# Performance work log

Hardware: AMD Instinct MI355X
Metric: run time of the kernel (lower is better)

Reference implementation:

```python
import jax, jax.numpy as jnp
import numpy as np

N = 50000      # nodes
EPS = 1e-5     # BatchNorm eps


def setup_inputs() -> dict:
    key = jax.random.key(0)
    ks = jax.random.split(key, 8)
    F_IN, H, C, E = 128, 128, 40, 600000
    x = jax.random.normal(ks[0], (N, F_IN), jnp.float32)
    edge_index = jax.random.randint(ks[1], (2, E), 0, N, dtype=jnp.int64)
    def glorot(k, fi, fo):
        s = np.sqrt(6.0 / (fi + fo)).astype(np.float32)
        return jax.random.uniform(k, (fi, fo), jnp.float32, -s, s)
    return {
        "x": x, "edge_index": edge_index,
        "W1": glorot(ks[2], F_IN, H), "b1": jnp.zeros((H,), jnp.float32),
        "gamma1": jnp.ones((H,), jnp.float32), "beta1": jnp.zeros((H,), jnp.float32),
        "W2": glorot(ks[3], H, H), "b2": jnp.zeros((H,), jnp.float32),
        "gamma2": jnp.ones((H,), jnp.float32), "beta2": jnp.zeros((H,), jnp.float32),
        "W3": glorot(ks[4], H, C), "b3": jnp.zeros((C,), jnp.float32),
    }


def _gcn_conv(x, W, b, src, dst, norm):
    # X' = D^-1/2 (A+I) D^-1/2 (X W) + b   (PyG GCNConv with self-loops)
    h = x @ W                               # [N, Fo]
    msg = h[src] * norm[:, None]            # [E+N, Fo] gather + scale
    out = jax.ops.segment_sum(msg, dst, num_segments=N)  # scatter-add
    return out + b


def _batchnorm(x, gamma, beta):
    # training-mode BatchNorm1d: batch stats over node axis, biased variance
    mu = jnp.mean(x, axis=0)
    var = jnp.mean(jnp.square(x - mu), axis=0)
    return (x - mu) * jax.lax.rsqrt(var + EPS) * gamma + beta


def reference(x, edge_index, W1, b1, gamma1, beta1, W2, b2, gamma2, beta2, W3, b3):
    loops = jnp.arange(N, dtype=edge_index.dtype)
    src = jnp.concatenate([edge_index[0], loops])
    dst = jnp.concatenate([edge_index[1], loops])
    deg = jax.ops.segment_sum(jnp.ones_like(dst, dtype=x.dtype), dst, num_segments=N)
    dinv = jax.lax.rsqrt(jnp.maximum(deg, 1.0))  # deg >= 1 due to self-loops
    norm = dinv[src] * dinv[dst]                 # [E+N]

    h = _gcn_conv(x, W1, b1, src, dst, norm)
    h = jax.nn.relu(_batchnorm(h, gamma1, beta1))
    h = _gcn_conv(h, W2, b2, src, dst, norm)
    h = jax.nn.relu(_batchnorm(h, gamma2, beta2))
    h = _gcn_conv(h, W3, b3, src, dst, norm)
    return jax.nn.log_softmax(h, axis=-1)
```

## Files before the change

kernel.cpp:

```cpp
#include <hip/hip_runtime.h>
#include <hip/hip_bf16.h>

#define EPS 1e-5f
#define SCAN_BLOCKS 256

typedef __attribute__((ext_vector_type(8))) short bf16x8;
typedef __attribute__((ext_vector_type(4))) float f32x4;

__device__ inline float bf2f(unsigned short u) {
    union { unsigned int i; float f; } v;
    v.i = ((unsigned int)u) << 16;
    return v.f;
}

__device__ inline unsigned short f2bf(float f) {
    union { float f; unsigned int i; } v;
    v.f = f;
    unsigned int x = v.i;
    unsigned int rounded = x + 0x7FFF + ((x >> 16) & 1);
    return (unsigned short)(rounded >> 16);
}


__global__ void count_kernel(const int* __restrict__ dst, int* __restrict__ counts, int e) {
    int i = blockIdx.x * blockDim.x + threadIdx.x;
    if (i < e) atomicAdd(&counts[dst[i]], 1);
}

__global__ __launch_bounds__(256) void scan_partial_kernel(const int* __restrict__ counts,
                                                           int* __restrict__ partials, int n) {
    __shared__ int sh[256];
    int chunk = (n + gridDim.x - 1) / gridDim.x;
    int lo = blockIdx.x * chunk;
    int hi = lo + chunk; if (hi > n) hi = n;
    int s = 0;
    for (int i = lo + threadIdx.x; i < hi; i += 256) s += counts[i];
    sh[threadIdx.x] = s;
    __syncthreads();
    for (int d = 128; d; d >>= 1) {
        if (threadIdx.x < d) sh[threadIdx.x] += sh[threadIdx.x + d];
        __syncthreads();
    }
    if (threadIdx.x == 0) partials[blockIdx.x] = sh[0];
}

__global__ __launch_bounds__(256) void scan_level2_kernel(int* __restrict__ partials) {
    __shared__ int sh[256];
    int t = threadIdx.x;
    sh[t] = partials[t];
    __syncthreads();
    for (int d = 1; d < 256; d <<= 1) {
        int v = (t >= d) ? sh[t - d] : 0;
        __syncthreads();
        sh[t] += v;
        __syncthreads();
    }
    partials[t] = (t == 0) ? 0 : sh[t - 1];
}

__global__ __launch_bounds__(256) void scan_write_kernel(const int* __restrict__ counts,
                                                         const int* __restrict__ partials,
                                                         int* __restrict__ offs,
                                                         float* __restrict__ dinv, int n) {
    __shared__ int sh[256];
    int t = threadIdx.x;
    int chunk = (n + gridDim.x - 1) / gridDim.x;
    int lo = blockIdx.x * chunk;
    int hi = lo + chunk; if (hi > n) hi = n;
    int per = (chunk + 255) / 256;
    int tlo = lo + t * per;
    int thi = tlo + per; if (thi > hi) thi = hi;
    int s = 0;
    for (int i = tlo; i < thi; ++i) s += counts[i];
    sh[t] = s;
    __syncthreads();
    for (int d = 1; d < 256; d <<= 1) {
        int v = (t >= d) ? sh[t - d] : 0;
        __syncthreads();
        sh[t] += v;
        __syncthreads();
    }
    int run = partials[blockIdx.x] + ((t == 0) ? 0 : sh[t - 1]);
    for (int i = tlo; i < thi; ++i) {
        offs[i] = run;
        run += counts[i];
        dinv[i] = rsqrtf((float)(counts[i] + 1));
    }
    if (tlo < n && thi == n) offs[n] = run;
}

__global__ void scatter_kernel(const int* __restrict__ src, const int* __restrict__ dst,
                               const int* __restrict__ offs, int* __restrict__ fill,
                               const float* __restrict__ dinv,
                               int* __restrict__ csr_col, float* __restrict__ csr_val, int e) {
    int i = blockIdx.x * blockDim.x + threadIdx.x;
    if (i >= e) return;
    int s = src[i], d = dst[i];
    int pos = offs[d] + atomicAdd(&fill[d], 1);
    csr_col[pos] = s;
    csr_val[pos] = dinv[s] * dinv[d];
}

__global__ void prep_weights_kernel(const float* __restrict__ W1, const float* __restrict__ W2,
                                    const float* __restrict__ W3,
                                    unsigned short* __restrict__ WT1,
                                    unsigned short* __restrict__ WT2,
                                    unsigned short* __restrict__ WT3) {
    int i = blockIdx.x * blockDim.x + threadIdx.x;
    if (i < 16384) {
        int col = i >> 7, k = i & 127;
        WT1[i] = f2bf(W1[k * 128 + col]);
    } else if (i < 32768) {
        int j = i - 16384;
        int col = j >> 7, k = j & 127;
        WT2[j] = f2bf(W2[k * 128 + col]);
    } else if (i < 32768 + 6144) {
        int j = i - 32768;
        int col = j >> 7, k = j & 127;
        WT3[j] = (col < 40) ? f2bf(W3[k * 40 + col]) : 0;
    }
}

template<bool BN>
__global__ __launch_bounds__(256) void gemm128_mfma_kernel(
    const float* __restrict__ A, const unsigned short* __restrict__ WT,
    const float* __restrict__ stats, const float* __restrict__ gamma,
    const float* __restrict__ beta, float invn,
    unsigned short* __restrict__ C, int n) {
    __shared__ unsigned short lW[128 * 128];
    __shared__ unsigned short lA[64 * 128];
    int tid = threadIdx.x;
    const uint4* wsrc = (const uint4*)WT;
#pragma unroll
    for (int it = 0; it < 8; ++it) {
        int idx = tid + it * 256;
        int byte = idx << 4;
        int dst = byte ^ (((byte >> 8) & 7) << 4);
        *(uint4*)((char*)lW + dst) = wsrc[idx];
    }
    int row0 = blockIdx.x * 64;
#pragma unroll
    for (int it = 0; it < 4; ++it) {
        int idx = tid + it * 256;
        int r = idx >> 4;
        int cc = (idx & 15) << 3;
        int gr = row0 + r; if (gr > n - 1) gr = n - 1;
        const float* ap = A + (size_t)gr * 128 + cc;
        float4 f0 = *(const float4*)ap;
        float4 f1 = *(const float4*)(ap + 4);
        float v[8] = {f0.x, f0.y, f0.z, f0.w, f1.x, f1.y, f1.z, f1.w};
        union { unsigned short u[8]; uint4 q; } t;
#pragma unroll
        for (int j = 0; j < 8; ++j) {
            float x = v[j];
            if (BN) {
                int c = cc + j;
                float mu = stats[c] * invn;
                float var = stats[128 + c] * invn - mu * mu;
                float sc = gamma[c] * rsqrtf(var + EPS);
                float sh = beta[c] - mu * sc;
                x = fmaf(x, sc, sh);
                x = x > 0.0f ? x : 0.0f;
            }
            t.u[j] = f2bf(x);
        }
        int byte = idx << 4;
        int dst = byte ^ (((byte >> 8) & 7) << 4);
        *(uint4*)((char*)lA + dst) = t.q;
    }
    __syncthreads();

    int lane = tid & 63;
    int mrow0 = (tid >> 6) << 4;
    int arow = mrow0 + (lane & 15);
    int swz = (lane & 7) << 4;
    int koff = (lane >> 4) << 4;
    const char* pA = (const char*)lA + (arow << 8);
    const char* pB = (const char*)lW + ((lane & 15) << 8);
    f32x4 acc[8];
#pragma unroll
    for (int t8 = 0; t8 < 8; ++t8) acc[t8] = (f32x4){0.f, 0.f, 0.f, 0.f};
#pragma unroll
    for (int kk = 0; kk < 4; ++kk) {
        int kb = (kk << 6) + koff;
        bf16x8 af = *(const bf16x8*)(pA + (kb ^ swz));
#pragma unroll
        for (int t8 = 0; t8 < 8; ++t8) {
            bf16x8 bf = *(const bf16x8*)(pB + (t8 << 12) + (kb ^ swz));
            acc[t8] = __builtin_amdgcn_mfma_f32_16x16x32_bf16(af, bf, acc[t8], 0, 0, 0);
        }
    }
    int crow = row0 + mrow0 + ((lane >> 4) << 2);
    int ccol = lane & 15;
    unsigned short* cp = C + (size_t)crow * 128 + ccol;
#pragma unroll
    for (int j = 0; j < 4; ++j) {
        if (crow + j < n) {
#pragma unroll
            for (int t8 = 0; t8 < 8; ++t8)
                cp[(size_t)j * 128 + t8 * 16] = f2bf(acc[t8][j]);
        }
    }
}

__global__ __launch_bounds__(256) void gemm40_lsm_mfma_kernel(
    const unsigned short* __restrict__ A, const unsigned short* __restrict__ WT,
    const float* __restrict__ b3, float* __restrict__ out, int n) {
    __shared__ unsigned short lW[48 * 128];
    __shared__ unsigned short lA[64 * 128];
    __shared__ float sRow[64 * 49];
    __shared__ float sD[64];
    __shared__ float sB[48];
    int tid = threadIdx.x;
    if (tid < 48) sB[tid] = (tid < 40) ? b3[tid] : 0.0f;
    const uint4* wsrc = (const uint4*)WT;
#pragma unroll
    for (int it = 0; it < 3; ++it) {
        int idx = tid + it * 256;
        int byte = idx << 4;
        int dst = byte ^ (((byte >> 8) & 7) << 4);
        *(uint4*)((char*)lW + dst) = wsrc[idx];
    }
    int row0 = blockIdx.x * 64;
#pragma unroll
    for (int it = 0; it < 4; ++it) {
        int idx = tid + it * 256;
        int r = idx >> 4;
        int cc = (idx & 15) << 3;
        int gr = row0 + r; if (gr > n - 1) gr = n - 1;
        uint4 q = *(const uint4*)(A + (size_t)gr * 128 + cc);
        int byte = idx << 4;
        int dst = byte ^ (((byte >> 8) & 7) << 4);
        *(uint4*)((char*)lA + dst) = q;
    }
    __syncthreads();

    int lane = tid & 63;
    int mrow0 = (tid >> 6) << 4;
    int arow = mrow0 + (lane & 15);
    int swz = (lane & 7) << 4;
    int koff = (lane >> 4) << 4;
    const char* pA = (const char*)lA + (arow << 8);
    const char* pB = (const char*)lW + ((lane & 15) << 8);
    f32x4 acc[3];
#pragma unroll
    for (int t8 = 0; t8 < 3; ++t8) acc[t8] = (f32x4){0.f, 0.f, 0.f, 0.f};
#pragma unroll
    for (int kk = 0; kk < 4; ++kk) {
        int kb = (kk << 6) + koff;
        bf16x8 af = *(const bf16x8*)(pA + (kb ^ swz));
#pragma unroll
        for (int t8 = 0; t8 < 3; ++t8) {
            bf16x8 bf = *(const bf16x8*)(pB + (t8 << 12) + (kb ^ swz));
            acc[t8] = __builtin_amdgcn_mfma_f32_16x16x32_bf16(af, bf, acc[t8], 0, 0, 0);
        }
    }
    int lrow = mrow0 + ((lane >> 4) << 2);
    int ccol = lane & 15;
#pragma unroll
    for (int t8 = 0; t8 < 3; ++t8)
#pragma unroll
        for (int j = 0; j < 4; ++j)
            sRow[(lrow + j) * 49 + t8 * 16 + ccol] = acc[t8][j] + sB[t8 * 16 + ccol];
    __syncthreads();
    if (tid < 64) {
        float m = -1e30f;
        for (int c = 0; c < 40; ++c) m = fmaxf(m, sRow[tid * 49 + c]);
        float l = 0.0f;
        for (int c = 0; c < 40; ++c) l += expf(sRow[tid * 49 + c] - m);
        sD[tid] = m + logf(l);
    }
    __syncthreads();
    for (int i = tid; i < 64 * 40; i += 256) {
        int r = i / 40;
        int c = i - r * 40;
        int gr = row0 + r;
        if (gr < n) out[(size_t)gr * 40 + c] = sRow[r * 49 + c] - sD[r];
    }
}


template<bool OUT16>
__global__ __launch_bounds__(256) void aggregate128_kernel(
    const unsigned short* __restrict__ H, const int* __restrict__ offs,
    const int* __restrict__ cols, const float* __restrict__ vals,
    const float* __restrict__ dinv, void* __restrict__ outp, int n) {
    int node = (blockIdx.x * blockDim.x + threadIdx.x) >> 6;
    if (node >= n) return;
    int lane = threadIdx.x & 63;
    float di = dinv[node];
    unsigned int h0 = *(const unsigned int*)(H + (size_t)node * 128 + lane * 2);
    float2 acc0, acc1;
    acc0.x = bf2f((unsigned short)h0) * di * di;
    acc0.y = bf2f((unsigned short)(h0 >> 16)) * di * di;
    acc1.x = 0.0f; acc1.y = 0.0f;
    int e0 = offs[node], e1 = offs[node + 1];
    int e = e0;
    for (; e + 2 <= e1; e += 2) {
        int sA = cols[e], sB = cols[e + 1];
        float wA = vals[e], wB = vals[e + 1];
        unsigned int hA = *(const unsigned int*)(H + (size_t)sA * 128 + lane * 2);
        unsigned int hB = *(const unsigned int*)(H + (size_t)sB * 128 + lane * 2);
        acc0.x += bf2f((unsigned short)hA) * wA;
        acc0.y += bf2f((unsigned short)(hA >> 16)) * wA;
        acc1.x += bf2f((unsigned short)hB) * wB;
        acc1.y += bf2f((unsigned short)(hB >> 16)) * wB;
    }
    if (e < e1) {
        int sA = cols[e];
        float wA = vals[e];
        unsigned int hA = *(const unsigned int*)(H + (size_t)sA * 128 + lane * 2);
        acc0.x += bf2f((unsigned short)hA) * wA;
        acc0.y += bf2f((unsigned short)(hA >> 16)) * wA;
    }
    acc0.x += acc1.x;
    acc0.y += acc1.y;
    if (OUT16) {
        unsigned int pack = (unsigned int)f2bf(acc0.x) | ((unsigned int)f2bf(acc0.y) << 16);
        *(unsigned int*)((unsigned short*)outp + (size_t)node * 128 + lane * 2) = pack;
    } else {
        *(float2*)((float*)outp + (size_t)node * 128 + lane * 2) = acc0;
    }
}


__global__ __launch_bounds__(256) void bn_stats_kernel(const float* __restrict__ X,
                                                       float* __restrict__ stats, int n) {
    int tid = threadIdx.x;
    int c = tid & 127;
    int r0 = blockIdx.x * 2 + (tid >> 7);
    float s = 0.0f, q = 0.0f;
    for (int r = r0; r < n; r += gridDim.x * 2) {
        float v = X[(size_t)r * 128 + c];
        s += v;
        q += v * v;
    }
    __shared__ float sh[256], shq[256];
    sh[tid] = s; shq[tid] = q;
    __syncthreads();
    if (tid < 128) {
        atomicAdd(&stats[c], sh[tid] + sh[tid + 128]);
        atomicAdd(&stats[128 + c], shq[tid] + shq[tid + 128]);
    }
}

__global__ void bn_apply_relu_bf16_kernel(const float* __restrict__ X,
                                          const float* __restrict__ stats,
                                          const float* __restrict__ gamma,
                                          const float* __restrict__ beta,
                                          unsigned short* __restrict__ Y, int n, float invn) {
    int i = blockIdx.x * blockDim.x + threadIdx.x;
    int total = n * 32;
    if (i >= total) return;
    int c0 = (i & 31) * 4;
    float4 x = ((const float4*)X)[i];
    float xv[4] = {x.x, x.y, x.z, x.w};
    ushort4 o;
    unsigned short ov[4];
#pragma unroll
    for (int j = 0; j < 4; ++j) {
        int c = c0 + j;
        float mu = stats[c] * invn;
        float var = stats[128 + c] * invn - mu * mu;
        float sc = gamma[c] * rsqrtf(var + EPS);
        float sh = beta[c] - mu * sc;
        float v = fmaf(xv[j], sc, sh);
        ov[j] = f2bf(v > 0.0f ? v : 0.0f);
    }
    o.x = ov[0]; o.y = ov[1]; o.z = ov[2]; o.w = ov[3];
    ((ushort4*)Y)[i] = o;
}


extern "C" void kernel_launch(void* const* d_in, const int* in_sizes, int n_in,
                              void* d_out, int out_size, void* d_ws, size_t ws_size,
                              hipStream_t stream) {
    const float* x   = (const float*)d_in[0];
    const int*   ei  = (const int*)d_in[1];
    const float* W1  = (const float*)d_in[2];
    const float* g1  = (const float*)d_in[4];
    const float* bt1 = (const float*)d_in[5];
    const float* W2  = (const float*)d_in[6];
    const float* g2  = (const float*)d_in[8];
    const float* bt2 = (const float*)d_in[9];
    const float* W3  = (const float*)d_in[10];
    const float* b3  = (const float*)d_in[11];

    int n = in_sizes[0] / 128;
    int e = in_sizes[1] / 2;
    const int* src = ei;
    const int* dst = ei + e;

    char* p = (char*)d_ws;
    auto alloc = [&](size_t bytes) -> char* {
        char* q = p;
        p += (bytes + 255) & ~(size_t)255;
        return q;
    };
    int*            counts   = (int*)alloc((size_t)n * 4);
    int*            offs     = (int*)alloc((size_t)(n + 1) * 4);
    int*            fill     = (int*)alloc((size_t)n * 4);
    float*          dinv     = (float*)alloc((size_t)n * 4);
    int*            partials = (int*)alloc(SCAN_BLOCKS * 4);
    int*            csr_col  = (int*)alloc((size_t)e * 4);
    float*          csr_val  = (float*)alloc((size_t)e * 4);
    float*          stats    = (float*)alloc(512 * 4);
    unsigned short* WT1      = (unsigned short*)alloc(16384 * 2);
    unsigned short* WT2      = (unsigned short*)alloc(16384 * 2);
    unsigned short* WT3      = (unsigned short*)alloc(6144 * 2);
    unsigned short* Hb       = (unsigned short*)alloc((size_t)n * 128 * 2);
    unsigned short* Hb2      = (unsigned short*)alloc((size_t)n * 128 * 2);
    float*          bufA     = (float*)alloc((size_t)n * 128 * 4);

    hipMemsetAsync(counts, 0, (size_t)n * 4, stream);
    hipMemsetAsync(fill, 0, (size_t)n * 4, stream);
    hipMemsetAsync(stats, 0, 512 * 4, stream);

    const int tb = 256;
    float invn = 1.0f / n;
    prep_weights_kernel<<<(38912 + tb - 1) / tb, tb, 0, stream>>>(W1, W2, W3, WT1, WT2, WT3);
    count_kernel<<<(e + tb - 1) / tb, tb, 0, stream>>>(dst, counts, e);
    scan_partial_kernel<<<SCAN_BLOCKS, tb, 0, stream>>>(counts, partials, n);
    scan_level2_kernel<<<1, tb, 0, stream>>>(partials);
    scan_write_kernel<<<SCAN_BLOCKS, tb, 0, stream>>>(counts, partials, offs, dinv, n);
    scatter_kernel<<<(e + tb - 1) / tb, tb, 0, stream>>>(src, dst, offs, fill, dinv,
                                                         csr_col, csr_val, e);

    int gblocks = (n + 63) / 64;
    int ablocks = (n + 3) / 4;

    gemm128_mfma_kernel<false><<<gblocks, tb, 0, stream>>>(x, WT1, nullptr, nullptr, nullptr,
                                                           0.0f, Hb, n);
    aggregate128_kernel<false><<<ablocks, tb, 0, stream>>>(Hb, offs, csr_col, csr_val, dinv,
                                                           bufA, n);
    bn_stats_kernel<<<256, tb, 0, stream>>>(bufA, stats, n);
    gemm128_mfma_kernel<true><<<gblocks, tb, 0, stream>>>(bufA, WT2, stats, g1, bt1, invn,
                                                          Hb, n);
    aggregate128_kernel<false><<<ablocks, tb, 0, stream>>>(Hb, offs, csr_col, csr_val, dinv,
                                                           bufA, n);
    bn_stats_kernel<<<256, tb, 0, stream>>>(bufA, stats + 256, n);
    bn_apply_relu_bf16_kernel<<<(n * 32 + tb - 1) / tb, tb, 0, stream>>>(bufA, stats + 256, g2,
                                                                         bt2, Hb, n, invn);
    aggregate128_kernel<true><<<ablocks, tb, 0, stream>>>(Hb, offs, csr_col, csr_val, dinv,
                                                          Hb2, n);
    gemm40_lsm_mfma_kernel<<<gblocks, tb, 0, stream>>>(Hb2, WT3, b3, (float*)d_out, n);
}
```

Before: 305.9 us.

## Store aggregates as bf16, fuse BN-apply into aggregation, pack CSR col/val

Aggregation outputs are now written as bf16 instead of fp32, which halves the intermediate traffic read by bn_stats and the GEMM. The second BN+ReLU is fused into the third aggregation's gather, so the separate bn_apply kernel is removed. CSR column and weight are packed into int2 so one load fetches both, and the gather loop is unrolled by four with more accumulators. The BN scale and shift are precomputed once per block in shared memory; the cost is BN statistics computed on bf16-rounded values and BN math repeated on every neighbour gather.

```diff
diff --git a/kernel.cpp b/kernel.cpp
--- a/kernel.cpp
+++ b/kernel.cpp
@@ -92,13 +92,13 @@
 __global__ void scatter_kernel(const int* __restrict__ src, const int* __restrict__ dst,
                                const int* __restrict__ offs, int* __restrict__ fill,
                                const float* __restrict__ dinv,
-                               int* __restrict__ csr_col, float* __restrict__ csr_val, int e) {
+                               int2* __restrict__ csr, int e) {
     int i = blockIdx.x * blockDim.x + threadIdx.x;
     if (i >= e) return;
     int s = src[i], d = dst[i];
     int pos = offs[d] + atomicAdd(&fill[d], 1);
-    csr_col[pos] = s;
-    csr_val[pos] = dinv[s] * dinv[d];
+    float w = dinv[s] * dinv[d];
+    csr[pos] = make_int2(s, __float_as_int(w));
 }
 
 __global__ void prep_weights_kernel(const float* __restrict__ W1, const float* __restrict__ W2,
@@ -121,15 +121,26 @@
     }
 }
 
-template<bool BN>
+template<int MODE>
 __global__ __launch_bounds__(256) void gemm128_mfma_kernel(
-    const float* __restrict__ A, const unsigned short* __restrict__ WT,
+    const void* __restrict__ Aptr, const unsigned short* __restrict__ WT,
     const float* __restrict__ stats, const float* __restrict__ gamma,
     const float* __restrict__ beta, float invn,
     unsigned short* __restrict__ C, int n) {
     __shared__ unsigned short lW[128 * 128];
     __shared__ unsigned short lA[64 * 128];
+    __shared__ float scs[128], shs[128];
     int tid = threadIdx.x;
+    if (MODE == 1) {
+        if (tid < 128) {
+            float mu = stats[tid] * invn;
+            float var = stats[128 + tid] * invn - mu * mu;
+            float sc = gamma[tid] * rsqrtf(var + EPS);
+            scs[tid] = sc;
+            shs[tid] = beta[tid] - mu * sc;
+        }
+        __syncthreads();
+    }
     const uint4* wsrc = (const uint4*)WT;
 #pragma unroll
     for (int it = 0; it < 8; ++it) {
@@ -145,24 +156,25 @@
         int r = idx >> 4;
         int cc = (idx & 15) << 3;
         int gr = row0 + r; if (gr > n - 1) gr = n - 1;
-        const float* ap = A + (size_t)gr * 128 + cc;
-        float4 f0 = *(const float4*)ap;
-        float4 f1 = *(const float4*)(ap + 4);
-        float v[8] = {f0.x, f0.y, f0.z, f0.w, f1.x, f1.y, f1.z, f1.w};
         union { unsigned short u[8]; uint4 q; } t;
-#pragma unroll
-        for (int j = 0; j < 8; ++j) {
-            float x = v[j];
-            if (BN) {
+        if (MODE == 0) {
+            const float* ap = (const float*)Aptr + (size_t)gr * 128 + cc;
+            float4 f0 = *(const float4*)ap;
+            float4 f1 = *(const float4*)(ap + 4);
+            float v[8] = {f0.x, f0.y, f0.z, f0.w, f1.x, f1.y, f1.z, f1.w};
+#pragma unroll
+            for (int j = 0; j < 8; ++j) t.u[j] = f2bf(v[j]);
+        } else {
+            uint4 q = *(const uint4*)((const unsigned short*)Aptr + (size_t)gr * 128 + cc);
+            unsigned int w[4] = {q.x, q.y, q.z, q.w};
+#pragma unroll
+            for (int j = 0; j < 8; ++j) {
+                float x = bf2f((unsigned short)(w[j >> 1] >> ((j & 1) * 16)));
                 int c = cc + j;
-                float mu = stats[c] * invn;
-                float var = stats[128 + c] * invn - mu * mu;
-                float sc = gamma[c] * rsqrtf(var + EPS);
-                float sh = beta[c] - mu * sc;
-                x = fmaf(x, sc, sh);
+                x = fmaf(x, scs[c], shs[c]);
                 x = x > 0.0f ? x : 0.0f;
+                t.u[j] = f2bf(x);
             }
-            t.u[j] = f2bf(x);
         }
         int byte = idx << 4;
         int dst = byte ^ (((byte >> 8) & 7) << 4);
@@ -280,58 +292,77 @@
 }
 
 
-template<bool OUT16>
+template<bool BN>
 __global__ __launch_bounds__(256) void aggregate128_kernel(
     const unsigned short* __restrict__ H, const int* __restrict__ offs,
-    const int* __restrict__ cols, const float* __restrict__ vals,
-    const float* __restrict__ dinv, void* __restrict__ outp, int n) {
+    const int2* __restrict__ csr, const float* __restrict__ dinv,
+    const float* __restrict__ stats, const float* __restrict__ gamma,
+    const float* __restrict__ beta, float invn,
+    unsigned short* __restrict__ out, int n) {
     int node = (blockIdx.x * blockDim.x + threadIdx.x) >> 6;
     if (node >= n) return;
     int lane = threadIdx.x & 63;
+    int c0 = lane * 2;
+    float sc0 = 1.0f, sh0 = 0.0f, sc1 = 1.0f, sh1 = 0.0f;
+    if (BN) {
+        float mu0 = stats[c0] * invn;
+        float var0 = stats[128 + c0] * invn - mu0 * mu0;
+        sc0 = gamma[c0] * rsqrtf(var0 + EPS);
+        sh0 = beta[c0] - mu0 * sc0;
+        float mu1 = stats[c0 + 1] * invn;
+        float var1 = stats[128 + c0 + 1] * invn - mu1 * mu1;
+        sc1 = gamma[c0 + 1] * rsqrtf(var1 + EPS);
+        sh1 = beta[c0 + 1] - mu1 * sc1;
+    }
+    auto loadf = [&](int row) -> float2 {
+        unsigned int hv = *(const unsigned int*)(H + (size_t)row * 128 + c0);
+        float x0 = bf2f((unsigned short)hv);
+        float x1 = bf2f((unsigned short)(hv >> 16));
+        if (BN) {
+            x0 = fmaf(x0, sc0, sh0); x0 = x0 > 0.0f ? x0 : 0.0f;
+            x1 = fmaf(x1, sc1, sh1); x1 = x1 > 0.0f ? x1 : 0.0f;
+        }
+        return make_float2(x0, x1);
+    };
     float di = dinv[node];
-    unsigned int h0 = *(const unsigned int*)(H + (size_t)node * 128 + lane * 2);
-    float2 acc0, acc1;
-    acc0.x = bf2f((unsigned short)h0) * di * di;
-    acc0.y = bf2f((unsigned short)(h0 >> 16)) * di * di;
-    acc1.x = 0.0f; acc1.y = 0.0f;
-    int e0 = offs[node], e1 = offs[node + 1];
-    int e = e0;
-    for (; e + 2 <= e1; e += 2) {
-        int sA = cols[e], sB = cols[e + 1];
-        float wA = vals[e], wB = vals[e + 1];
-        unsigned int hA = *(const unsigned int*)(H + (size_t)sA * 128 + lane * 2);
-        unsigned int hB = *(const unsigned int*)(H + (size_t)sB * 128 + lane * 2);
-        acc0.x += bf2f((unsigned short)hA) * wA;
-        acc0.y += bf2f((unsigned short)(hA >> 16)) * wA;
-        acc1.x += bf2f((unsigned short)hB) * wB;
-        acc1.y += bf2f((unsigned short)(hB >> 16)) * wB;
-    }
-    if (e < e1) {
-        int sA = cols[e];
-        float wA = vals[e];
-        unsigned int hA = *(const unsigned int*)(H + (size_t)sA * 128 + lane * 2);
-        acc0.x += bf2f((unsigned short)hA) * wA;
-        acc0.y += bf2f((unsigned short)(hA >> 16)) * wA;
-    }
-    acc0.x += acc1.x;
-    acc0.y += acc1.y;
-    if (OUT16) {
-        unsigned int pack = (unsigned int)f2bf(acc0.x) | ((unsigned int)f2bf(acc0.y) << 16);
-        *(unsigned int*)((unsigned short*)outp + (size_t)node * 128 + lane * 2) = pack;
-    } else {
-        *(float2*)((float*)outp + (size_t)node * 128 + lane * 2) = acc0;
-    }
-}
-
-
-__global__ __launch_bounds__(256) void bn_stats_kernel(const float* __restrict__ X,
+    float2 self = loadf(node);
+    float2 a0 = make_float2(self.x * di * di, self.y * di * di);
+    float2 a1 = make_float2(0.f, 0.f), a2 = make_float2(0.f, 0.f), a3 = make_float2(0.f, 0.f);
+    int e = offs[node], e1 = offs[node + 1];
+    for (; e + 4 <= e1; e += 4) {
+        int2 q0 = csr[e], q1 = csr[e + 1], q2 = csr[e + 2], q3 = csr[e + 3];
+        float2 h0 = loadf(q0.x);
+        float2 h1 = loadf(q1.x);
+        float2 h2 = loadf(q2.x);
+        float2 h3 = loadf(q3.x);
+        float w0 = __int_as_float(q0.y), w1 = __int_as_float(q1.y);
+        float w2 = __int_as_float(q2.y), w3 = __int_as_float(q3.y);
+        a0.x = fmaf(h0.x, w0, a0.x); a0.y = fmaf(h0.y, w0, a0.y);
+        a1.x = fmaf(h1.x, w1, a1.x); a1.y = fmaf(h1.y, w1, a1.y);
+        a2.x = fmaf(h2.x, w2, a2.x); a2.y = fmaf(h2.y, w2, a2.y);
+        a3.x = fmaf(h3.x, w3, a3.x); a3.y = fmaf(h3.y, w3, a3.y);
+    }
+    for (; e < e1; ++e) {
+        int2 q = csr[e];
+        float2 h = loadf(q.x);
+        float w = __int_as_float(q.y);
+        a0.x = fmaf(h.x, w, a0.x); a0.y = fmaf(h.y, w, a0.y);
+    }
+    float rx = (a0.x + a1.x) + (a2.x + a3.x);
+    float ry = (a0.y + a1.y) + (a2.y + a3.y);
+    unsigned int pack = (unsigned int)f2bf(rx) | ((unsigned int)f2bf(ry) << 16);
+    *(unsigned int*)(out + (size_t)node * 128 + c0) = pack;
+}
+
+
+__global__ __launch_bounds__(256) void bn_stats_kernel(const unsigned short* __restrict__ X,
                                                        float* __restrict__ stats, int n) {
     int tid = threadIdx.x;
     int c = tid & 127;
     int r0 = blockIdx.x * 2 + (tid >> 7);
     float s = 0.0f, q = 0.0f;
     for (int r = r0; r < n; r += gridDim.x * 2) {
-        float v = X[(size_t)r * 128 + c];
+        float v = bf2f(X[(size_t)r * 128 + c]);
         s += v;
         q += v * v;
     }
@@ -342,33 +373,6 @@
         atomicAdd(&stats[c], sh[tid] + sh[tid + 128]);
         atomicAdd(&stats[128 + c], shq[tid] + shq[tid + 128]);
     }
-}
-
-__global__ void bn_apply_relu_bf16_kernel(const float* __restrict__ X,
-                                          const float* __restrict__ stats,
-                                          const float* __restrict__ gamma,
-                                          const float* __restrict__ beta,
-                                          unsigned short* __restrict__ Y, int n, float invn) {
-    int i = blockIdx.x * blockDim.x + threadIdx.x;
-    int total = n * 32;
-    if (i >= total) return;
-    int c0 = (i & 31) * 4;
-    float4 x = ((const float4*)X)[i];
-    float xv[4] = {x.x, x.y, x.z, x.w};
-    ushort4 o;
-    unsigned short ov[4];
-#pragma unroll
-    for (int j = 0; j < 4; ++j) {
-        int c = c0 + j;
-        float mu = stats[c] * invn;
-        float var = stats[128 + c] * invn - mu * mu;
-        float sc = gamma[c] * rsqrtf(var + EPS);
-        float sh = beta[c] - mu * sc;
-        float v = fmaf(xv[j], sc, sh);
-        ov[j] = f2bf(v > 0.0f ? v : 0.0f);
-    }
-    o.x = ov[0]; o.y = ov[1]; o.z = ov[2]; o.w = ov[3];
-    ((ushort4*)Y)[i] = o;
 }
 
 
@@ -402,15 +406,15 @@
     int*            fill     = (int*)alloc((size_t)n * 4);
     float*          dinv     = (float*)alloc((size_t)n * 4);
     int*            partials = (int*)alloc(SCAN_BLOCKS * 4);
-    int*            csr_col  = (int*)alloc((size_t)e * 4);
-    float*          csr_val  = (float*)alloc((size_t)e * 4);
+    int2*           csr      = (int2*)alloc((size_t)e * 8);
     float*          stats    = (float*)alloc(512 * 4);
     unsigned short* WT1      = (unsigned short*)alloc(16384 * 2);
     unsigned short* WT2      = (unsigned short*)alloc(16384 * 2);
     unsigned short* WT3      = (unsigned short*)alloc(6144 * 2);
     unsigned short* Hb       = (unsigned short*)alloc((size_t)n * 128 * 2);
+    unsigned short* Ab       = (unsigned short*)alloc((size_t)n * 128 * 2);
+    unsigned short* Ab2      = (unsigned short*)alloc((size_t)n * 128 * 2);
     unsigned short* Hb2      = (unsigned short*)alloc((size_t)n * 128 * 2);
-    float*          bufA     = (float*)alloc((size_t)n * 128 * 4);
 
     hipMemsetAsync(counts, 0, (size_t)n * 4, stream);
     hipMemsetAsync(fill, 0, (size_t)n * 4, stream);
@@ -423,25 +427,21 @@
     scan_partial_kernel<<<SCAN_BLOCKS, tb, 0, stream>>>(counts, partials, n);
     scan_level2_kernel<<<1, tb, 0, stream>>>(partials);
     scan_write_kernel<<<SCAN_BLOCKS, tb, 0, stream>>>(counts, partials, offs, dinv, n);
-    scatter_kernel<<<(e + tb - 1) / tb, tb, 0, stream>>>(src, dst, offs, fill, dinv,
-                                                         csr_col, csr_val, e);
+    scatter_kernel<<<(e + tb - 1) / tb, tb, 0, stream>>>(src, dst, offs, fill, dinv, csr, e);
 
     int gblocks = (n + 63) / 64;
     int ablocks = (n + 3) / 4;
 
-    gemm128_mfma_kernel<false><<<gblocks, tb, 0, stream>>>(x, WT1, nullptr, nullptr, nullptr,
-                                                           0.0f, Hb, n);
-    aggregate128_kernel<false><<<ablocks, tb, 0, stream>>>(Hb, offs, csr_col, csr_val, dinv,
-                                                           bufA, n);
-    bn_stats_kernel<<<256, tb, 0, stream>>>(bufA, stats, n);
-    gemm128_mfma_kernel<true><<<gblocks, tb, 0, stream>>>(bufA, WT2, stats, g1, bt1, invn,
-                                                          Hb, n);
-    aggregate128_kernel<false><<<ablocks, tb, 0, stream>>>(Hb, offs, csr_col, csr_val, dinv,
-                                                           bufA, n);
-    bn_stats_kernel<<<256, tb, 0, stream>>>(bufA, stats + 256, n);
-    bn_apply_relu_bf16_kernel<<<(n * 32 + tb - 1) / tb, tb, 0, stream>>>(bufA, stats + 256, g2,
-                                                                         bt2, Hb, n, invn);
-    aggregate128_kernel<true><<<ablocks, tb, 0, stream>>>(Hb, offs, csr_col, csr_val, dinv,
-                                                          Hb2, n);
+    gemm128_mfma_kernel<0><<<gblocks, tb, 0, stream>>>(x, WT1, nullptr, nullptr, nullptr,
+                                                       0.0f, Hb, n);
+    aggregate128_kernel<false><<<ablocks, tb, 0, stream>>>(Hb, offs, csr, dinv, nullptr,
+                                                           nullptr, nullptr, 0.0f, Ab, n);
+    bn_stats_kernel<<<256, tb, 0, stream>>>(Ab, stats, n);
+    gemm128_mfma_kernel<1><<<gblocks, tb, 0, stream>>>(Ab, WT2, stats, g1, bt1, invn, Hb, n);
+    aggregate128_kernel<false><<<ablocks, tb, 0, stream>>>(Hb, offs, csr, dinv, nullptr,
+                                                           nullptr, nullptr, 0.0f, Ab2, n);
+    bn_stats_kernel<<<256, tb, 0, stream>>>(Ab2, stats + 256, n);
+    aggregate128_kernel<true><<<ablocks, tb, 0, stream>>>(Ab2, offs, csr, dinv, stats + 256,
+                                                          g2, bt2, invn, Hb2, n);
     gemm40_lsm_mfma_kernel<<<gblocks, tb, 0, stream>>>(Hb2, WT3, b3, (float*)d_out, n);
 }
```

New measurement: 269.1 us. -12.0%, faster.
